# Performance work log

Measured on AMD Instinct MI355X. Metric: run time of the kernel, lower is better.

## Reference

```python
import jax, jax.numpy as jnp
import numpy as np

B, TX, DA, DS, H = 64, 2048, 256, 256, 50

def setup_inputs() -> dict:
    key = jax.random.key(0)
    k1, k2, k3, k4 = jax.random.split(key, 4)
    a = jax.random.normal(k1, (B, TX, DA), dtype=jnp.float32)
    s = jax.random.normal(k2, (B, DS), dtype=jnp.float32)
    # Dense(50, relu) params on concat dim (DA+DS)
    W1 = jax.random.normal(k3, (DA + DS, H), dtype=jnp.float32) / np.sqrt(DA + DS)
    b1 = jnp.zeros((H,), dtype=jnp.float32)
    # Dense(1, tanh) params
    W2 = jax.random.normal(k4, (H, 1), dtype=jnp.float32) / np.sqrt(H)
    b2 = jnp.zeros((1,), dtype=jnp.float32)
    return {"a": a, "s": s, "W1": W1, "b1": b1, "W2": W2, "b2": b2}

def reference(a, s, W1, b1, W2, b2):
    # repeat s along time: [B, Tx, Ds]
    s_rep = jnp.broadcast_to(s[:, None, :], (a.shape[0], a.shape[1], s.shape[-1]))
    x = jnp.concatenate([a, s_rep], axis=-1)              # [B, Tx, Da+Ds]
    h = jax.nn.relu(jnp.einsum('btc,ch->bth', x, W1) + b1)  # [B, Tx, 50]
    e = jnp.tanh(jnp.einsum('bth,ho->bto', h, W2) + b2)     # [B, Tx, 1]
    alphas = jax.nn.softmax(e, axis=1)                     # softmax over time
    # Dot(axes=1): contract the time axis -> [B, 1, Da]
    context = jnp.einsum('bto,btd->bod', alphas, a)
    return context
```

## Files before the change

kernel.cpp:

```cpp
#include <hip/hip_runtime.h>

#define B_ 64
#define TX_ 2048
#define DA_ 256
#define DS_ 256
#define H_ 50

typedef __attribute__((ext_vector_type(4))) float f32x4;
typedef __attribute__((ext_vector_type(8))) short short8;

__device__ __forceinline__ unsigned short f2bf(float x) {
  unsigned int u = __builtin_bit_cast(unsigned int, x);
  u += 0x7FFFu + ((u >> 16) & 1u);
  return (unsigned short)(u >> 16);
}
__device__ __forceinline__ float bf2f(unsigned short h) {
  unsigned int u = ((unsigned int)h) << 16;
  return __builtin_bit_cast(float, u);
}
__device__ __forceinline__ unsigned bitf(float x) {
  return __builtin_bit_cast(unsigned, x);
}
__device__ __forceinline__ unsigned pack_hi(float x, float y) {
  return __builtin_amdgcn_perm(bitf(y), bitf(x), 0x07060302);
}
__device__ __forceinline__ float trunc_bf(float x) {
  return __builtin_bit_cast(float, bitf(x) & 0xFFFF0000u);
}

#define WS_NUM 0
#define WS_DEN 16384
#define WS_C   16448
#define WS_W2  20544
#define WS_B   20608

__global__ __launch_bounds__(256) void prep_kernel(
    const float* __restrict__ s, const float* __restrict__ W1,
    const float* __restrict__ b1, const float* __restrict__ W2,
    float* __restrict__ ws)
{
  const int blk = blockIdx.x;
  const int t = threadIdx.x;
  unsigned short* wsB = (unsigned short*)(ws + WS_B);

  if (blk < 64) {
    const int b = blk;
    ws[WS_NUM + b * 256 + t] = 0.0f;
    if (t == 0) ws[WS_DEN + b] = 0.0f;

    const int h4 = t >> 2, kq = t & 3;
    float cp = 0.0f;
    if (h4 < H_) {
      const float* srow = s + b * DS_;
      #pragma unroll 8
      for (int k = kq * 64; k < kq * 64 + 64; ++k)
        cp += srow[k] * W1[(size_t)(DA_ + k) * H_ + h4];
    }
    cp += __shfl_down(cp, 1);
    cp += __shfl_down(cp, 2);
    if (kq == 0) ws[WS_C + b * 64 + h4] = (h4 < H_) ? (cp + b1[h4]) : 0.0f;
    if (b == 0 && t < 64) ws[WS_W2 + t] = (t < H_) ? W2[t] : 0.0f;
  } else {
    const int idx = (blk - 64) * 256 + t;
    const int j = idx & 7;
    const int l = (idx >> 3) & 63;
    const int nt = (idx >> 9) & 3;
    const int term = (idx >> 11) & 1;
    const int c = idx >> 12;
    const int k = c * 32 + (l >> 4) * 8 + j;
    const int n = nt * 16 + (l & 15);
    const float wv = (n < H_) ? W1[(size_t)k * H_ + n] : 0.0f;
    const unsigned short hi = f2bf(wv);
    const unsigned short val = term == 0 ? hi : f2bf(wv - bf2f(hi));
    wsB[((size_t)((c * 2 + term) * 4 + nt)) * 512 + l * 8 + j] = val;
  }
}

__global__ __launch_bounds__(256, 2) void fused_kernel(
    const float* __restrict__ a, const float* __restrict__ ws_f,
    const float* __restrict__ b2, float* __restrict__ num,
    float* __restrict__ den)
{
  __shared__ float tile[16384];
  __shared__ float w_sh[64];

  const int t = threadIdx.x;
  const int l = t & 63;
  const int w = __builtin_amdgcn_readfirstlane(t >> 6);
  const int blk = blockIdx.x;
  const int b = blk >> 5;
  const long R0 = (long)blk * 64;

  const unsigned short* wsB = (const unsigned short*)(ws_f + WS_B);

  #define STAGE(c)                                                             \
    {                                                                          \
      _Pragma("unroll")                                                        \
      for (int i = 0; i < 2; ++i) {                                            \
        const int slot = w * 2 + i;                                            \
        const long gbyte = (R0 + slot * 8 + (l >> 3)) * 1024 + (c) * 128 +     \
                           (((l & 7) ^ ((l >> 3) & 7)) * 16);                  \
        __builtin_amdgcn_global_load_lds(                                      \
            (const __attribute__((address_space(1))) void*)((const char*)a +   \
                                                            gbyte),            \
            (__attribute__((address_space(3))) void*)&tile[(c)*2048 +          \
                                                           slot * 256],        \
            16, 0, 0);                                                         \
      }                                                                        \
    }

  STAGE(0);
  STAGE(1);

  short8 Bh[2][4], Bl[2][4];
  {
    const short8* Bp = (const short8*)wsB;
    #pragma unroll
    for (int nt = 0; nt < 4; ++nt) {
      Bh[0][nt] = Bp[nt * 64 + l];
      Bl[0][nt] = Bp[(4 + nt) * 64 + l];
    }
  }

  f32x4 acc[4];
  #pragma unroll
  for (int nt = 0; nt < 4; ++nt) acc[nt] = (f32x4){0.f, 0.f, 0.f, 0.f};

  const int row = w * 16 + (l & 15);
  const int mask = (l & 7) << 4;
  const int obase = (l >> 4) * 32;

  #pragma unroll
  for (int c = 0; c < 8; ++c) {
    if (c + 2 < 8) STAGE(c + 2);
    if (c + 1 < 8) {
      const short8* Bp = (const short8*)(wsB + (size_t)(c + 1) * 4096);
      #pragma unroll
      for (int nt = 0; nt < 4; ++nt) {
        Bh[(c + 1) & 1][nt] = Bp[nt * 64 + l];
        Bl[(c + 1) & 1][nt] = Bp[(4 + nt) * 64 + l];
      }
    }
    if (c < 6)       asm volatile("s_waitcnt vmcnt(10)" ::: "memory");
    else if (c == 6) asm volatile("s_waitcnt vmcnt(8)" ::: "memory");
    else             asm volatile("s_waitcnt vmcnt(0)" ::: "memory");
    __builtin_amdgcn_sched_barrier(0);

    const char* tb = (const char*)tile + (size_t)c * 8192 + row * 128;
    const float4 v0 = *(const float4*)(tb + (obase ^ mask));
    const float4 v1 = *(const float4*)(tb + ((obase + 16) ^ mask));
    const float av[8] = {v0.x, v0.y, v0.z, v0.w, v1.x, v1.y, v1.z, v1.w};

    unsigned hu[4], lu[4];
    #pragma unroll
    for (int p = 0; p < 4; ++p) {
      const float x = av[2 * p], y = av[2 * p + 1];
      hu[p] = pack_hi(x, y);
      lu[p] = pack_hi(x - trunc_bf(x), y - trunc_bf(y));
    }
    const short8 Ah = __builtin_bit_cast(short8, *(uint4*)hu);
    const short8 Al = __builtin_bit_cast(short8, *(uint4*)lu);

    #pragma unroll
    for (int nt = 0; nt < 4; ++nt) {
      acc[nt] = __builtin_amdgcn_mfma_f32_16x16x32_bf16(Ah, Bh[c & 1][nt], acc[nt], 0, 0, 0);
      acc[nt] = __builtin_amdgcn_mfma_f32_16x16x32_bf16(Ah, Bl[c & 1][nt], acc[nt], 0, 0, 0);
      acc[nt] = __builtin_amdgcn_mfma_f32_16x16x32_bf16(Al, Bh[c & 1][nt], acc[nt], 0, 0, 0);
    }
  }
  #undef STAGE

  float cv[4], w2v[4];
  #pragma unroll
  for (int nt = 0; nt < 4; ++nt) {
    const int n = nt * 16 + (l & 15);
    cv[nt] = ws_f[WS_C + b * 64 + n];
    w2v[nt] = ws_f[WS_W2 + n];
  }
  const float b2v = b2[0];

  #pragma unroll
  for (int r = 0; r < 4; ++r) {
    float e = 0.0f;
    #pragma unroll
    for (int nt = 0; nt < 4; ++nt)
      e += fmaxf(acc[nt][r] + cv[nt], 0.0f) * w2v[nt];
    e += __shfl_xor(e, 1);
    e += __shfl_xor(e, 2);
    e += __shfl_xor(e, 4);
    e += __shfl_xor(e, 8);
    e += b2v;
    const float th = 1.0f - 2.0f / (__expf(2.0f * e) + 1.0f);
    if ((l & 15) == 0) w_sh[w * 16 + (l >> 4) * 4 + r] = __expf(th);
  }
  __syncthreads();

  if (t < 64) {
    float v = w_sh[t];
    #pragma unroll
    for (int off = 32; off > 0; off >>= 1) v += __shfl_xor(v, off);
    if (t == 0) atomicAdd(&den[b], v);
  }

  {
    const int cc = t >> 5, col = t & 31;
    const char* tb = (const char*)tile + (size_t)cc * 8192;
    float sum = 0.0f;
    #pragma unroll 8
    for (int r = 0; r < 64; ++r) {
      const float av = *(const float*)(tb + r * 128 + ((col * 4) ^ ((r & 7) << 4)));
      sum += w_sh[r] * av;
    }
    atomicAdd(&num[b * 256 + t], sum);
  }
}

__global__ __launch_bounds__(256) void finish_kernel(
    const float* __restrict__ ws_f, float* __restrict__ out)
{
  const int b = blockIdx.x;
  const int t = threadIdx.x;
  out[b * 256 + t] = ws_f[WS_NUM + b * 256 + t] / ws_f[WS_DEN + b];
}

extern "C" void kernel_launch(void* const* d_in, const int* in_sizes, int n_in,
                              void* d_out, int out_size, void* d_ws, size_t ws_size,
                              hipStream_t stream) {
  const float* a  = (const float*)d_in[0];
  const float* s  = (const float*)d_in[1];
  const float* W1 = (const float*)d_in[2];
  const float* b1 = (const float*)d_in[3];
  const float* W2 = (const float*)d_in[4];
  const float* b2 = (const float*)d_in[5];
  float* out = (float*)d_out;
  float* ws  = (float*)d_ws;

  prep_kernel<<<dim3(192), dim3(256), 0, stream>>>(s, W1, b1, W2, ws);
  fused_kernel<<<dim3(2048), dim3(256), 0, stream>>>(
      a, ws, b2, ws + WS_NUM, ws + WS_DEN);
  finish_kernel<<<dim3(B_), dim3(256), 0, stream>>>(ws, out);
}
```

Measured before the change: 53.34 us.

## Shrink LDS to a four-slot ring and compute context from global reloads

Replaces the 64 KB per-block tile holding all eight column chunks with a four-slot ring buffer, and raises launch bounds from 2 to 4 blocks per CU. With the tile no longer fully resident, the final weighted sum re-reads rows of `a` from global memory, which should mostly hit cache. Each wave reduces its own 16 rows into a small LDS partial array, and those partials are summed before the atomics. The wait counts were not rescaled to the deeper prefetch, so they stay conservative and may block on loads that could still be in flight. The extra global re-reads also add memory traffic.

```diff
diff --git a/kernel.cpp b/kernel.cpp
--- a/kernel.cpp
+++ b/kernel.cpp
@@ -76,13 +76,13 @@
   }
 }
 
-__global__ __launch_bounds__(256, 2) void fused_kernel(
+__global__ __launch_bounds__(256, 4) void fused_kernel(
     const float* __restrict__ a, const float* __restrict__ ws_f,
     const float* __restrict__ b2, float* __restrict__ num,
     float* __restrict__ den)
 {
-  __shared__ float tile[16384];
-  __shared__ float w_sh[64];
+  __shared__ float ring[4][2048];
+  __shared__ float partial[4][256];
 
   const int t = threadIdx.x;
   const int l = t & 63;
@@ -103,14 +103,15 @@
         __builtin_amdgcn_global_load_lds(                                      \
             (const __attribute__((address_space(1))) void*)((const char*)a +   \
                                                             gbyte),            \
-            (__attribute__((address_space(3))) void*)&tile[(c)*2048 +          \
-                                                           slot * 256],        \
+            (__attribute__((address_space(3))) void*)&ring[(c) & 3]            \
+                                                         [slot * 256],         \
             16, 0, 0);                                                         \
       }                                                                        \
     }
 
   STAGE(0);
   STAGE(1);
+  STAGE(2);
 
   short8 Bh[2][4], Bl[2][4];
   {
@@ -132,7 +133,7 @@
 
   #pragma unroll
   for (int c = 0; c < 8; ++c) {
-    if (c + 2 < 8) STAGE(c + 2);
+    if (c + 3 < 8) STAGE(c + 3);
     if (c + 1 < 8) {
       const short8* Bp = (const short8*)(wsB + (size_t)(c + 1) * 4096);
       #pragma unroll
@@ -141,12 +142,12 @@
         Bl[(c + 1) & 1][nt] = Bp[(4 + nt) * 64 + l];
       }
     }
-    if (c < 6)       asm volatile("s_waitcnt vmcnt(10)" ::: "memory");
-    else if (c == 6) asm volatile("s_waitcnt vmcnt(8)" ::: "memory");
+    if (c <= 4)      asm volatile("s_waitcnt vmcnt(10)" ::: "memory");
+    else if (c <= 6) asm volatile("s_waitcnt vmcnt(8)" ::: "memory");
     else             asm volatile("s_waitcnt vmcnt(0)" ::: "memory");
     __builtin_amdgcn_sched_barrier(0);
 
-    const char* tb = (const char*)tile + (size_t)c * 8192 + row * 128;
+    const char* tb = (const char*)&ring[c & 3][0] + row * 128;
     const float4 v0 = *(const float4*)(tb + (obase ^ mask));
     const float4 v1 = *(const float4*)(tb + ((obase + 16) ^ mask));
     const float av[8] = {v0.x, v0.y, v0.z, v0.w, v1.x, v1.y, v1.z, v1.w};
@@ -179,6 +180,7 @@
   }
   const float b2v = b2[0];
 
+  float wr[4];
   #pragma unroll
   for (int r = 0; r < 4; ++r) {
     float e = 0.0f;
@@ -191,27 +193,29 @@
     e += __shfl_xor(e, 8);
     e += b2v;
     const float th = 1.0f - 2.0f / (__expf(2.0f * e) + 1.0f);
-    if ((l & 15) == 0) w_sh[w * 16 + (l >> 4) * 4 + r] = __expf(th);
-  }
+    wr[r] = __expf(th);
+  }
+
+  f32x4 csum = (f32x4){0.f, 0.f, 0.f, 0.f};
+  float wsum = 0.0f;
+  const float* arow2 = a + (R0 + w * 16) * DA_ + 4 * l;
+  #pragma unroll 4
+  for (int r = 0; r < 16; ++r) {
+    const float wv = __shfl(wr[r & 3], (r >> 2) * 16);
+    wsum += wv;
+    const float4 av = *(const float4*)(arow2 + (size_t)r * DA_);
+    csum.x += wv * av.x;
+    csum.y += wv * av.y;
+    csum.z += wv * av.z;
+    csum.w += wv * av.w;
+  }
+  if (l == 0) atomicAdd(&den[b], wsum);
+  *(f32x4*)&partial[w][4 * l] = csum;
   __syncthreads();
 
-  if (t < 64) {
-    float v = w_sh[t];
-    #pragma unroll
-    for (int off = 32; off > 0; off >>= 1) v += __shfl_xor(v, off);
-    if (t == 0) atomicAdd(&den[b], v);
-  }
-
   {
-    const int cc = t >> 5, col = t & 31;
-    const char* tb = (const char*)tile + (size_t)cc * 8192;
-    float sum = 0.0f;
-    #pragma unroll 8
-    for (int r = 0; r < 64; ++r) {
-      const float av = *(const float*)(tb + r * 128 + ((col * 4) ^ ((r & 7) << 4)));
-      sum += w_sh[r] * av;
-    }
-    atomicAdd(&num[b * 256 + t], sum);
+    const float v = partial[0][t] + partial[1][t] + partial[2][t] + partial[3][t];
+    atomicAdd(&num[b * 256 + t], v);
   }
 }
 
```

After: 102.7 us. +92.6%, slower.
